# Kernel optimization log

Hardware: AMD Instinct MI355X
Metric: run time of the kernel (lower is better)

Reference implementation:

```python
import jax, jax.numpy as jnp
import numpy as np

B, DL, DC, DG = 4, 64, 64, 64
NL, NC = 8192, 16384
SLOPE = 0.01  # LeakyReLU default negative_slope


def _lin(x, W, b):
    # 1x1 Conv1d == per-node linear: x [B, in, N] -> [B, out, N]
    return jnp.einsum('oi,bin->bon', W, x) + b[None, :, None]


def _leaky(x):
    return jnp.where(x >= 0, x, SLOPE * x)


def _flip(L):
    # swap first and second half along last dim (literal <-> complement)
    n = L.shape[-1]
    return jnp.concatenate([L[..., n // 2:], L[..., :n // 2]], axis=-1)


def setup_inputs() -> dict:
    key = jax.random.key(0)
    ks = jax.random.split(key, 14)
    L_t = jax.random.normal(ks[0], (B, DL, NL), dtype=jnp.float32)
    C_t = jax.random.normal(ks[1], (B, DC, NC), dtype=jnp.float32)
    U_t = jax.random.normal(ks[2], (B, DG, 1), dtype=jnp.float32)
    # sparse 0/1 adjacency, ~8 literals per clause
    A = (jax.random.uniform(ks[3], (NC, NL)) < 0.001).astype(jnp.float32)
    A_t = A.T
    s = 0.05
    W_Lmsg = s * jax.random.normal(ks[4], (DC, DL));      b_Lmsg = jnp.zeros((DC,))
    W_Cmsg = s * jax.random.normal(ks[5], (DL, DC));      b_Cmsg = jnp.zeros((DL,))
    W_Lu   = s * jax.random.normal(ks[6], (DL, 3 * DL));  b_Lu   = jnp.zeros((DL,))
    W_Cu   = s * jax.random.normal(ks[7], (DC, 2 * DC));  b_Cu   = jnp.zeros((DC,))
    W_Uu   = s * jax.random.normal(ks[8], (DG, DL + DC + DG)); b_Uu = jnp.zeros((DG,))
    return dict(L_t=L_t, C_t=C_t, U_t=U_t, A=A, A_t=A_t,
                W_Lmsg=W_Lmsg, b_Lmsg=b_Lmsg, W_Cmsg=W_Cmsg, b_Cmsg=b_Cmsg,
                W_Lu=W_Lu, b_Lu=b_Lu, W_Cu=W_Cu, b_Cu=b_Cu, W_Uu=W_Uu, b_Uu=b_Uu)


def reference(L_t, C_t, U_t, A, A_t,
              W_Lmsg, b_Lmsg, W_Cmsg, b_Cmsg,
              W_Lu, b_Lu, W_Cu, b_Cu, W_Uu, b_Uu):
    # literal -> clause messages: [B, d_c, n_lits] @ [n_lits, n_clauses]
    M_l = _lin(L_t, W_Lmsg, b_Lmsg) @ A_t
    C_t_new = _leaky(_lin(jnp.concatenate([C_t, M_l], axis=1), W_Cu, b_Cu))
    # clause -> literal messages: [B, d_l, n_clauses] @ [n_clauses, n_lits]
    M_c = _lin(C_t_new, W_Cmsg, b_Cmsg) @ A
    L_t_new = _leaky(_lin(jnp.concatenate([L_t, M_c, _flip(L_t)], axis=1), W_Lu, b_Lu))
    glob = jnp.concatenate([L_t_new.sum(-1, keepdims=True),
                            C_t_new.sum(-1, keepdims=True), U_t], axis=1)
    U_t_new = _leaky(_lin(glob, W_Uu, b_Uu))
    return (L_t_new, C_t_new, U_t_new)
```

## Files before the change

### kernel.cpp

```cpp
#include <hip/hip_runtime.h>

#define NLIT 8192
#define NCLS 16384
#define DD 64
#define CCAP 64
#define LCAP 64

__device__ __forceinline__ float leaky(float x){ return x >= 0.f ? x : 0.01f*x; }

__device__ __forceinline__ int sel4(int g, int4 li){
  return g==0 ? li.x : (g==1 ? li.y : (g==2 ? li.z : li.w));
}

__device__ __forceinline__ float bf2f(unsigned short u){
  unsigned v = ((unsigned)u) << 16;
  union { unsigned u; float f; } c; c.u = v; return c.f;
}
__device__ __forceinline__ unsigned short f2bf(float f){
  union { float f; unsigned u; } c; c.f = f;
  unsigned b = c.u + 0x7fffu + ((c.u >> 16) & 1u);
  return (unsigned short)(b >> 16);
}

__global__ __launch_bounds__(256) void extract_lmsg_k(const uint4* __restrict__ A4,
    int* __restrict__ ccnt, int* __restrict__ clist,
    int* __restrict__ lcnt, int* __restrict__ llist,
    const float* __restrict__ L, const float* __restrict__ W,
    const float* __restrict__ bias, unsigned short* __restrict__ LmsgT){
  if (blockIdx.x < 16384){
    const int T = 16384*256;
    int tid = blockIdx.x*256 + threadIdx.x;
    uint4 v[8];
    #pragma unroll
    for (int u=0;u<8;u++) v[u] = A4[tid + (size_t)u*T];
    #pragma unroll
    for (int u=0;u<8;u++){
      if (v[u].x | v[u].y | v[u].z | v[u].w){
        int i = tid + u*T;
        int c = i >> 11;
        int l = (i & 2047) << 2;
        unsigned vv[4] = {v[u].x, v[u].y, v[u].z, v[u].w};
        #pragma unroll
        for (int j=0;j<4;j++){
          if (vv[j]){
            int p = atomicAdd(&ccnt[c],1);
            if (p < CCAP) clist[c*CCAP+p] = l+j;
            int q = atomicAdd(&lcnt[l+j],1);
            if (q < LCAP) llist[(l+j)*LCAP+q] = c;
          }
        }
      }
    }
  } else {
    __shared__ float X[64][65];
    __shared__ float Y[64][65];
    int bid = blockIdx.x - 16384;
    int b   = (bid & 7) >> 1;
    int l0  = (((bid >> 3) << 1) | (bid & 1)) << 6;
    int lane = threadIdx.x & 63;
    int wg = __builtin_amdgcn_readfirstlane(threadIdx.x >> 6);
    const float* Lb = L + (size_t)b*DD*NLIT;
    #pragma unroll
    for (int r=0;r<16;r++){
      int i = wg + 4*r;
      X[lane][i] = Lb[(size_t)i*NLIT + l0 + lane];
    }
    __syncthreads();
    float acc[16];
    #pragma unroll
    for (int j=0;j<16;j++) acc[j] = bias[wg*16+j];
    #pragma unroll 4
    for (int i=0;i<64;i++){
      float x = X[lane][i];
      #pragma unroll
      for (int j=0;j<16;j++) acc[j] += W[(wg*16+j)*64+i] * x;
    }
    #pragma unroll
    for (int j=0;j<16;j++) Y[lane][wg*16+j] = acc[j];
    __syncthreads();
    unsigned short* out = LmsgT + ((size_t)b*NLIT + l0)*64;
    #pragma unroll
    for (int r=0;r<16;r++){
      int cc = wg + 4*r;
      out[cc*64 + lane] = f2bf(Y[cc][lane]);
    }
  }
}

__device__ __forceinline__ void gather_grp4(const unsigned short* __restrict__ src,
    const int* __restrict__ list, int cap, const int* kk, int lane,
    float (* __restrict__ sb)[65], int row0){
  int g = lane >> 4;
  int h = lane & 15;
  float4 a0={0.f,0.f,0.f,0.f}, a1=a0, a2=a0, a3=a0;
  int r0=(kk[0]+3)>>2, r1=(kk[1]+3)>>2, r2=(kk[2]+3)>>2, r3=(kk[3]+3)>>2;
  int Rm = max(max(r0,r1),max(r2,r3));
  for (int r=0;r<Rm;r++){
    if (r<r0){ int4 li=*(const int4*)&list[0*cap+4*r]; int e=4*r+g; bool vd=e<kk[0];
      int idx=vd?sel4(g,li):0; ushort4 x=*(const ushort4*)&src[(size_t)idx*64+4*h];
      if(vd){ a0.x+=bf2f(x.x); a0.y+=bf2f(x.y); a0.z+=bf2f(x.z); a0.w+=bf2f(x.w); } }
    if (r<r1){ int4 li=*(const int4*)&list[1*cap+4*r]; int e=4*r+g; bool vd=e<kk[1];
      int idx=vd?sel4(g,li):0; ushort4 x=*(const ushort4*)&src[(size_t)idx*64+4*h];
      if(vd){ a1.x+=bf2f(x.x); a1.y+=bf2f(x.y); a1.z+=bf2f(x.z); a1.w+=bf2f(x.w); } }
    if (r<r2){ int4 li=*(const int4*)&list[2*cap+4*r]; int e=4*r+g; bool vd=e<kk[2];
      int idx=vd?sel4(g,li):0; ushort4 x=*(const ushort4*)&src[(size_t)idx*64+4*h];
      if(vd){ a2.x+=bf2f(x.x); a2.y+=bf2f(x.y); a2.z+=bf2f(x.z); a2.w+=bf2f(x.w); } }
    if (r<r3){ int4 li=*(const int4*)&list[3*cap+4*r]; int e=4*r+g; bool vd=e<kk[3];
      int idx=vd?sel4(g,li):0; ushort4 x=*(const ushort4*)&src[(size_t)idx*64+4*h];
      if(vd){ a3.x+=bf2f(x.x); a3.y+=bf2f(x.y); a3.z+=bf2f(x.z); a3.w+=bf2f(x.w); } }
  }
  #pragma unroll
  for (int s=16;s<=32;s<<=1){
    a0.x+=__shfl_xor(a0.x,s,64); a0.y+=__shfl_xor(a0.y,s,64); a0.z+=__shfl_xor(a0.z,s,64); a0.w+=__shfl_xor(a0.w,s,64);
    a1.x+=__shfl_xor(a1.x,s,64); a1.y+=__shfl_xor(a1.y,s,64); a1.z+=__shfl_xor(a1.z,s,64); a1.w+=__shfl_xor(a1.w,s,64);
    a2.x+=__shfl_xor(a2.x,s,64); a2.y+=__shfl_xor(a2.y,s,64); a2.z+=__shfl_xor(a2.z,s,64); a2.w+=__shfl_xor(a2.w,s,64);
    a3.x+=__shfl_xor(a3.x,s,64); a3.y+=__shfl_xor(a3.y,s,64); a3.z+=__shfl_xor(a3.z,s,64); a3.w+=__shfl_xor(a3.w,s,64);
  }
  sb[row0+0][4*h+g] = g==0?a0.x:(g==1?a0.y:(g==2?a0.z:a0.w));
  sb[row0+1][4*h+g] = g==0?a1.x:(g==1?a1.y:(g==2?a1.z:a1.w));
  sb[row0+2][4*h+g] = g==0?a2.x:(g==1?a2.y:(g==2?a2.z:a2.w));
  sb[row0+3][4*h+g] = g==0?a3.x:(g==1?a3.y:(g==2?a3.z:a3.w));
}

__global__ __launch_bounds__(512) void clause_k(const float* __restrict__ Ct,
    const unsigned short* __restrict__ LmsgT, const int* __restrict__ ccnt, const int* __restrict__ clist,
    const float* __restrict__ W_Cu, const float* __restrict__ b_Cu,
    const float* __restrict__ W_Cmsg, const float* __restrict__ b_Cmsg,
    unsigned short* __restrict__ CmsgT, float* __restrict__ outC){
  __shared__ float SA[64][65];
  __shared__ float SB[64][65];
  int bx = blockIdx.x;
  int b  = (bx & 7) >> 1;
  int c0 = (((bx >> 3) << 1) | (bx & 1)) << 6;
  int lane = threadIdx.x & 63;
  int wg = __builtin_amdgcn_readfirstlane(threadIdx.x >> 6);
  int kk[8];
  #pragma unroll
  for (int t=0;t<8;t++){
    int k = ccnt[c0 + wg*8 + t];
    kk[t] = k > CCAP ? CCAP : k;
  }
  const float* Cb = Ct + (size_t)b*DD*NCLS;
  #pragma unroll
  for (int r=0;r<8;r++){
    int i = wg + 8*r;
    SA[lane][i] = Cb[(size_t)i*NCLS + c0 + lane];
  }
  const unsigned short* Lm = LmsgT + (size_t)b*NLIT*64;
  #pragma unroll
  for (int tg=0;tg<2;tg++){
    int row0 = wg*8 + tg*4;
    gather_grp4(Lm, &clist[(c0+row0)*CCAP], CCAP, &kk[tg*4], lane, SB, row0);
  }
  __syncthreads();
  float v[8];
  {
    float acc[8];
    #pragma unroll
    for (int j=0;j<8;j++) acc[j] = b_Cu[wg*8+j];
    #pragma unroll 4
    for (int i=0;i<64;i++){
      float xa = SA[lane][i];
      float xm = SB[lane][i];
      #pragma unroll
      for (int j=0;j<8;j++){
        int o = wg*8+j;
        acc[j] += W_Cu[o*128+i]*xa + W_Cu[o*128+64+i]*xm;
      }
    }
    #pragma unroll
    for (int j=0;j<8;j++) v[j] = leaky(acc[j]);
  }
  float* oC = outC + (size_t)b*DD*NCLS;
  #pragma unroll
  for (int j=0;j<8;j++){
    int o = wg*8+j;
    oC[(size_t)o*NCLS + c0 + lane] = v[j];
  }
  __syncthreads();
  #pragma unroll
  for (int j=0;j<8;j++) SB[lane][wg*8+j] = v[j];
  __syncthreads();
  float acc2[8];
  #pragma unroll
  for (int j=0;j<8;j++) acc2[j] = b_Cmsg[wg*8+j];
  #pragma unroll 4
  for (int i=0;i<64;i++){
    float x = SB[lane][i];
    #pragma unroll
    for (int j=0;j<8;j++) acc2[j] += W_Cmsg[(wg*8+j)*64+i]*x;
  }
  #pragma unroll
  for (int j=0;j<8;j++) SA[lane][wg*8+j] = acc2[j];
  __syncthreads();
  unsigned short* oM = CmsgT + ((size_t)b*NCLS + c0)*64;
  #pragma unroll
  for (int r=0;r<8;r++){
    int cc = wg + 8*r;
    oM[cc*64 + lane] = f2bf(SA[cc][lane]);
  }
}

__global__ __launch_bounds__(512) void literal_redc_k(const float* __restrict__ Lt,
    const unsigned short* __restrict__ CmsgT, const int* __restrict__ lcnt, const int* __restrict__ llist,
    const float* __restrict__ W_Lu, const float* __restrict__ b_Lu,
    float* __restrict__ outL, const float* __restrict__ outC, float* __restrict__ Csum){
  if (blockIdx.x >= 512){
    __shared__ float red[8];
    int r = blockIdx.x - 512;
    int t = threadIdx.x;
    float s = 0.f;
    const float4* p = (const float4*)(outC + (size_t)r*NCLS);
    #pragma unroll
    for (int i=0;i<8;i++){
      float4 v = p[t + 512*i];
      s += v.x + v.y + v.z + v.w;
    }
    #pragma unroll
    for (int sft=32;sft>0;sft>>=1) s += __shfl_xor(s, sft, 64);
    if ((t & 63) == 0) red[t >> 6] = s;
    __syncthreads();
    if (t == 0){
      float tot = 0.f;
      #pragma unroll
      for (int i=0;i<8;i++) tot += red[i];
      Csum[r] = tot;
    }
    return;
  }
  __shared__ float SX[64][65];
  __shared__ float SF[64][65];
  __shared__ float SM[64][65];
  int bx = blockIdx.x;
  int b  = (bx & 7) >> 1;
  int l0 = (((bx >> 3) << 1) | (bx & 1)) << 6;
  int lane = threadIdx.x & 63;
  int wg = __builtin_amdgcn_readfirstlane(threadIdx.x >> 6);
  int kk[8];
  #pragma unroll
  for (int t=0;t<8;t++){
    int k = lcnt[l0 + wg*8 + t];
    kk[t] = k > LCAP ? LCAP : k;
  }
  const float* Lb = Lt + (size_t)b*DD*NLIT;
  int f0 = l0 ^ 4096;
  #pragma unroll
  for (int r=0;r<8;r++){
    int i = wg + 8*r;
    SX[lane][i] = Lb[(size_t)i*NLIT + l0 + lane];
    SF[lane][i] = Lb[(size_t)i*NLIT + f0 + lane];
  }
  const unsigned short* Cm = CmsgT + (size_t)b*NCLS*64;
  #pragma unroll
  for (int tg=0;tg<2;tg++){
    int row0 = wg*8 + tg*4;
    gather_grp4(Cm, &llist[(l0+row0)*LCAP], LCAP, &kk[tg*4], lane, SM, row0);
  }
  __syncthreads();
  float acc[8];
  #pragma unroll
  for (int j=0;j<8;j++) acc[j] = b_Lu[wg*8+j];
  #pragma unroll 4
  for (int i=0;i<64;i++){
    float xx = SX[lane][i], xm = SM[lane][i], xf = SF[lane][i];
    #pragma unroll
    for (int j=0;j<8;j++){
      int o = wg*8+j;
      acc[j] += W_Lu[o*192+i]*xx + W_Lu[o*192+64+i]*xm + W_Lu[o*192+128+i]*xf;
    }
  }
  float* oL = outL + (size_t)b*DD*NLIT;
  #pragma unroll
  for (int j=0;j<8;j++){
    int o = wg*8+j;
    oL[(size_t)o*NLIT + l0 + lane] = leaky(acc[j]);
  }
}

__global__ __launch_bounds__(256) void redl_k(const float* __restrict__ outL,
    float* __restrict__ Lsum){
  __shared__ float red[4];
  int r = blockIdx.x;
  int t = threadIdx.x;
  float s = 0.f;
  const float4* p = (const float4*)(outL + (size_t)r*NLIT);
  #pragma unroll
  for (int i=0;i<8;i++){
    float4 v = p[t + 256*i];
    s += v.x + v.y + v.z + v.w;
  }
  #pragma unroll
  for (int sft=32;sft>0;sft>>=1) s += __shfl_xor(s, sft, 64);
  if ((t & 63) == 0) red[t >> 6] = s;
  __syncthreads();
  if (t == 0) Lsum[r] = red[0] + red[1] + red[2] + red[3];
}

__global__ void u_k(const float* __restrict__ Lsum, const float* __restrict__ Csum,
                    const float* __restrict__ Ut, const float* __restrict__ W,
                    const float* __restrict__ bias, float* __restrict__ outU){
  int t = threadIdx.x;
  int b = t >> 6, o = t & 63;
  float acc = bias[o];
  for (int i=0;i<64;i++){
    acc += W[o*192+i]*Lsum[b*64+i] + W[o*192+64+i]*Csum[b*64+i] + W[o*192+128+i]*Ut[b*64+i];
  }
  outU[t] = leaky(acc);
}

extern "C" void kernel_launch(void* const* d_in, const int* in_sizes, int n_in,
                              void* d_out, int out_size, void* d_ws, size_t ws_size,
                              hipStream_t stream){
  (void)in_sizes; (void)n_in; (void)out_size; (void)ws_size;
  const float* L_t    = (const float*)d_in[0];
  const float* C_t    = (const float*)d_in[1];
  const float* U_t    = (const float*)d_in[2];
  const float* A      = (const float*)d_in[3];
  const float* W_Lmsg = (const float*)d_in[5];
  const float* b_Lmsg = (const float*)d_in[6];
  const float* W_Cmsg = (const float*)d_in[7];
  const float* b_Cmsg = (const float*)d_in[8];
  const float* W_Lu   = (const float*)d_in[9];
  const float* b_Lu   = (const float*)d_in[10];
  const float* W_Cu   = (const float*)d_in[11];
  const float* b_Cu   = (const float*)d_in[12];
  const float* W_Uu   = (const float*)d_in[13];
  const float* b_Uu   = (const float*)d_in[14];

  char* ws = (char*)d_ws;
  unsigned short* LmsgT = (unsigned short*)ws;
  unsigned short* CmsgT = (unsigned short*)(ws + 4194304);
  int*   ccnt  = (int*)  (ws + 12582912);
  int*   lcnt  = (int*)  (ws + 12648448);
  float* Lsum  = (float*)(ws + 12681216);
  float* Csum  = (float*)(ws + 12682240);
  int*   clist = (int*)  (ws + 12683264);
  int*   llist = (int*)  (ws + 16877568);

  hipMemsetAsync(ws + 12582912, 0, 98304, stream);

  float* outL = (float*)d_out;
  float* outC = (float*)d_out + 2097152;
  float* outU = (float*)d_out + 6291456;

  extract_lmsg_k<<<16896, 256, 0, stream>>>((const uint4*)A, ccnt, clist, lcnt, llist,
                                            L_t, W_Lmsg, b_Lmsg, LmsgT);
  clause_k      <<<1024,  512, 0, stream>>>(C_t, LmsgT, ccnt, clist, W_Cu, b_Cu,
                                            W_Cmsg, b_Cmsg, CmsgT, outC);
  literal_redc_k<<<768,   512, 0, stream>>>(L_t, CmsgT, lcnt, llist, W_Lu, b_Lu,
                                            outL, outC, Csum);
  redl_k        <<<256,   256, 0, stream>>>(outL, Lsum);
  u_k           <<<1,     256, 0, stream>>>(Lsum, Csum, U_t, W_Uu, b_Uu, outU);
}
```

Before: 1.044 ms.

## Interleave batch dimension into message buffers so gathers fetch all batches at once

The literal and clause message buffers change from batch-major [B][N][64] to node-major [N][B*64]. Each neighbour index now fetches one contiguous 512-byte row covering all four batches, so every wave reads each adjacency list once instead of once per batch, and the loads are wide and coalesced. The clause and literal kernels are retiled to match: 32 clauses or 16 literals across all batches per block, with matching shared-memory layouts. Clause-side gathered sums are now kept in shared memory as bf16, which adds an extra rounding step.

```diff
diff --git a/kernel.cpp b/kernel.cpp
--- a/kernel.cpp
+++ b/kernel.cpp
@@ -8,13 +8,8 @@
 
 __device__ __forceinline__ float leaky(float x){ return x >= 0.f ? x : 0.01f*x; }
 
-__device__ __forceinline__ int sel4(int g, int4 li){
-  return g==0 ? li.x : (g==1 ? li.y : (g==2 ? li.z : li.w));
-}
-
 __device__ __forceinline__ float bf2f(unsigned short u){
-  unsigned v = ((unsigned)u) << 16;
-  union { unsigned u; float f; } c; c.u = v; return c.f;
+  union { unsigned u; float f; } c; c.u = ((unsigned)u) << 16; return c.f;
 }
 __device__ __forceinline__ unsigned short f2bf(float f){
   union { float f; unsigned u; } c; c.f = f;
@@ -26,7 +21,7 @@
     int* __restrict__ ccnt, int* __restrict__ clist,
     int* __restrict__ lcnt, int* __restrict__ llist,
     const float* __restrict__ L, const float* __restrict__ W,
-    const float* __restrict__ bias, unsigned short* __restrict__ LmsgT){
+    const float* __restrict__ bias, unsigned short* __restrict__ LmsgT2){
   if (blockIdx.x < 16384){
     const int T = 16384*256;
     int tid = blockIdx.x*256 + threadIdx.x;
@@ -55,8 +50,8 @@
     __shared__ float X[64][65];
     __shared__ float Y[64][65];
     int bid = blockIdx.x - 16384;
-    int b   = (bid & 7) >> 1;
-    int l0  = (((bid >> 3) << 1) | (bid & 1)) << 6;
+    int b   = bid >> 7;
+    int l0  = (bid & 127) << 6;
     int lane = threadIdx.x & 63;
     int wg = __builtin_amdgcn_readfirstlane(threadIdx.x >> 6);
     const float* Lb = L + (size_t)b*DD*NLIT;
@@ -78,131 +73,130 @@
     #pragma unroll
     for (int j=0;j<16;j++) Y[lane][wg*16+j] = acc[j];
     __syncthreads();
-    unsigned short* out = LmsgT + ((size_t)b*NLIT + l0)*64;
     #pragma unroll
     for (int r=0;r<16;r++){
       int cc = wg + 4*r;
-      out[cc*64 + lane] = f2bf(Y[cc][lane]);
-    }
-  }
-}
-
-__device__ __forceinline__ void gather_grp4(const unsigned short* __restrict__ src,
-    const int* __restrict__ list, int cap, const int* kk, int lane,
-    float (* __restrict__ sb)[65], int row0){
-  int g = lane >> 4;
-  int h = lane & 15;
-  float4 a0={0.f,0.f,0.f,0.f}, a1=a0, a2=a0, a3=a0;
-  int r0=(kk[0]+3)>>2, r1=(kk[1]+3)>>2, r2=(kk[2]+3)>>2, r3=(kk[3]+3)>>2;
-  int Rm = max(max(r0,r1),max(r2,r3));
-  for (int r=0;r<Rm;r++){
-    if (r<r0){ int4 li=*(const int4*)&list[0*cap+4*r]; int e=4*r+g; bool vd=e<kk[0];
-      int idx=vd?sel4(g,li):0; ushort4 x=*(const ushort4*)&src[(size_t)idx*64+4*h];
-      if(vd){ a0.x+=bf2f(x.x); a0.y+=bf2f(x.y); a0.z+=bf2f(x.z); a0.w+=bf2f(x.w); } }
-    if (r<r1){ int4 li=*(const int4*)&list[1*cap+4*r]; int e=4*r+g; bool vd=e<kk[1];
-      int idx=vd?sel4(g,li):0; ushort4 x=*(const ushort4*)&src[(size_t)idx*64+4*h];
-      if(vd){ a1.x+=bf2f(x.x); a1.y+=bf2f(x.y); a1.z+=bf2f(x.z); a1.w+=bf2f(x.w); } }
-    if (r<r2){ int4 li=*(const int4*)&list[2*cap+4*r]; int e=4*r+g; bool vd=e<kk[2];
-      int idx=vd?sel4(g,li):0; ushort4 x=*(const ushort4*)&src[(size_t)idx*64+4*h];
-      if(vd){ a2.x+=bf2f(x.x); a2.y+=bf2f(x.y); a2.z+=bf2f(x.z); a2.w+=bf2f(x.w); } }
-    if (r<r3){ int4 li=*(const int4*)&list[3*cap+4*r]; int e=4*r+g; bool vd=e<kk[3];
-      int idx=vd?sel4(g,li):0; ushort4 x=*(const ushort4*)&src[(size_t)idx*64+4*h];
-      if(vd){ a3.x+=bf2f(x.x); a3.y+=bf2f(x.y); a3.z+=bf2f(x.z); a3.w+=bf2f(x.w); } }
-  }
-  #pragma unroll
-  for (int s=16;s<=32;s<<=1){
-    a0.x+=__shfl_xor(a0.x,s,64); a0.y+=__shfl_xor(a0.y,s,64); a0.z+=__shfl_xor(a0.z,s,64); a0.w+=__shfl_xor(a0.w,s,64);
-    a1.x+=__shfl_xor(a1.x,s,64); a1.y+=__shfl_xor(a1.y,s,64); a1.z+=__shfl_xor(a1.z,s,64); a1.w+=__shfl_xor(a1.w,s,64);
-    a2.x+=__shfl_xor(a2.x,s,64); a2.y+=__shfl_xor(a2.y,s,64); a2.z+=__shfl_xor(a2.z,s,64); a2.w+=__shfl_xor(a2.w,s,64);
-    a3.x+=__shfl_xor(a3.x,s,64); a3.y+=__shfl_xor(a3.y,s,64); a3.z+=__shfl_xor(a3.z,s,64); a3.w+=__shfl_xor(a3.w,s,64);
-  }
-  sb[row0+0][4*h+g] = g==0?a0.x:(g==1?a0.y:(g==2?a0.z:a0.w));
-  sb[row0+1][4*h+g] = g==0?a1.x:(g==1?a1.y:(g==2?a1.z:a1.w));
-  sb[row0+2][4*h+g] = g==0?a2.x:(g==1?a2.y:(g==2?a2.z:a2.w));
-  sb[row0+3][4*h+g] = g==0?a3.x:(g==1?a3.y:(g==2?a3.z:a3.w));
+      LmsgT2[(size_t)(l0+cc)*256 + b*64 + lane] = f2bf(Y[cc][lane]);
+    }
+  }
 }
 
 __global__ __launch_bounds__(512) void clause_k(const float* __restrict__ Ct,
-    const unsigned short* __restrict__ LmsgT, const int* __restrict__ ccnt, const int* __restrict__ clist,
+    const unsigned short* __restrict__ LmsgT2, const int* __restrict__ ccnt,
+    const int* __restrict__ clist,
     const float* __restrict__ W_Cu, const float* __restrict__ b_Cu,
     const float* __restrict__ W_Cmsg, const float* __restrict__ b_Cmsg,
-    unsigned short* __restrict__ CmsgT, float* __restrict__ outC){
-  __shared__ float SA[64][65];
-  __shared__ float SB[64][65];
-  int bx = blockIdx.x;
-  int b  = (bx & 7) >> 1;
-  int c0 = (((bx >> 3) << 1) | (bx & 1)) << 6;
+    unsigned short* __restrict__ CmsgT2, float* __restrict__ outC){
+  __shared__ float SA[4][64][33];
+  __shared__ unsigned short SB[4][32][66];
+  int c0 = blockIdx.x << 5;
   int lane = threadIdx.x & 63;
-  int wg = __builtin_amdgcn_readfirstlane(threadIdx.x >> 6);
-  int kk[8];
-  #pragma unroll
-  for (int t=0;t<8;t++){
-    int k = ccnt[c0 + wg*8 + t];
-    kk[t] = k > CCAP ? CCAP : k;
-  }
-  const float* Cb = Ct + (size_t)b*DD*NCLS;
-  #pragma unroll
-  for (int r=0;r<8;r++){
-    int i = wg + 8*r;
-    SA[lane][i] = Cb[(size_t)i*NCLS + c0 + lane];
-  }
-  const unsigned short* Lm = LmsgT + (size_t)b*NLIT*64;
-  #pragma unroll
-  for (int tg=0;tg<2;tg++){
-    int row0 = wg*8 + tg*4;
-    gather_grp4(Lm, &clist[(c0+row0)*CCAP], CCAP, &kk[tg*4], lane, SB, row0);
-  }
-  __syncthreads();
-  float v[8];
-  {
-    float acc[8];
-    #pragma unroll
-    for (int j=0;j<8;j++) acc[j] = b_Cu[wg*8+j];
+  int w = __builtin_amdgcn_readfirstlane(threadIdx.x >> 6);
+  #pragma unroll
+  for (int it=0; it<16; it++){
+    int row = w*32 + it*2 + (lane>>5);
+    int b = row >> 6, i = row & 63;
+    SA[b][i][lane&31] = Ct[((size_t)b*64 + i)*NCLS + c0 + (lane&31)];
+  }
+  {
+    int kk[4], rT[4];
+    #pragma unroll
+    for (int t=0;t<4;t++){
+      int k = ccnt[c0 + w*4 + t];
+      kk[t] = k > CCAP ? CCAP : k;
+      rT[t] = (kk[t]+3) >> 2;
+    }
+    int Rm = max(max(rT[0],rT[1]),max(rT[2],rT[3]));
+    float4 acc[4];
+    #pragma unroll
+    for (int t=0;t<4;t++) acc[t] = make_float4(0.f,0.f,0.f,0.f);
+    for (int r=0;r<Rm;r++){
+      #pragma unroll
+      for (int t=0;t<4;t++){
+        if (r < rT[t]){
+          int4 li = *(const int4*)&clist[(c0 + w*4 + t)*CCAP + 4*r];
+          int idx[4] = {li.x, li.y, li.z, li.w};
+          #pragma unroll
+          for (int e=0;e<4;e++){
+            if (4*r+e < kk[t]){
+              ushort4 x = *(const ushort4*)&LmsgT2[(size_t)idx[e]*256 + 4*lane];
+              acc[t].x += bf2f(x.x); acc[t].y += bf2f(x.y);
+              acc[t].z += bf2f(x.z); acc[t].w += bf2f(x.w);
+            }
+          }
+        }
+      }
+    }
+    int b = lane >> 4, h = lane & 15;
+    #pragma unroll
+    for (int t=0;t<4;t++){
+      SB[b][w*4+t][4*h+0] = f2bf(acc[t].x);
+      SB[b][w*4+t][4*h+1] = f2bf(acc[t].y);
+      SB[b][w*4+t][4*h+2] = f2bf(acc[t].z);
+      SB[b][w*4+t][4*h+3] = f2bf(acc[t].w);
+    }
+  }
+  __syncthreads();
+  int b = w >> 1, half = w & 1, cl = lane & 31, sub = lane >> 5;
+  float acc[16];
+  {
+    int ob = half*32 + sub*16;
+    #pragma unroll
+    for (int j=0;j<16;j++) acc[j] = b_Cu[ob+j];
     #pragma unroll 4
     for (int i=0;i<64;i++){
-      float xa = SA[lane][i];
-      float xm = SB[lane][i];
-      #pragma unroll
-      for (int j=0;j<8;j++){
-        int o = wg*8+j;
+      float xa = SA[b][i][cl];
+      float xm = bf2f(SB[b][cl][i]);
+      #pragma unroll
+      for (int j=0;j<16;j++){
+        int o = ob + j;
         acc[j] += W_Cu[o*128+i]*xa + W_Cu[o*128+64+i]*xm;
       }
     }
     #pragma unroll
-    for (int j=0;j<8;j++) v[j] = leaky(acc[j]);
-  }
-  float* oC = outC + (size_t)b*DD*NCLS;
-  #pragma unroll
-  for (int j=0;j<8;j++){
-    int o = wg*8+j;
-    oC[(size_t)o*NCLS + c0 + lane] = v[j];
-  }
-  __syncthreads();
-  #pragma unroll
-  for (int j=0;j<8;j++) SB[lane][wg*8+j] = v[j];
-  __syncthreads();
-  float acc2[8];
-  #pragma unroll
-  for (int j=0;j<8;j++) acc2[j] = b_Cmsg[wg*8+j];
-  #pragma unroll 4
-  for (int i=0;i<64;i++){
-    float x = SB[lane][i];
-    #pragma unroll
-    for (int j=0;j<8;j++) acc2[j] += W_Cmsg[(wg*8+j)*64+i]*x;
-  }
-  #pragma unroll
-  for (int j=0;j<8;j++) SA[lane][wg*8+j] = acc2[j];
-  __syncthreads();
-  unsigned short* oM = CmsgT + ((size_t)b*NCLS + c0)*64;
-  #pragma unroll
-  for (int r=0;r<8;r++){
-    int cc = wg + 8*r;
-    oM[cc*64 + lane] = f2bf(SA[cc][lane]);
+    for (int j=0;j<16;j++) acc[j] = leaky(acc[j]);
+    float* oC = outC + (size_t)b*DD*NCLS;
+    #pragma unroll
+    for (int j=0;j<16;j++) oC[(size_t)(ob+j)*NCLS + c0 + cl] = acc[j];
+  }
+  __syncthreads();
+  {
+    int ob = half*32 + sub*16;
+    #pragma unroll
+    for (int j=0;j<16;j++) SA[b][ob+j][cl] = acc[j];
+  }
+  __syncthreads();
+  float acc2[16];
+  {
+    int ob = half*32 + sub*16;
+    #pragma unroll
+    for (int j=0;j<16;j++) acc2[j] = b_Cmsg[ob+j];
+    #pragma unroll 4
+    for (int i=0;i<64;i++){
+      float x = SA[b][i][cl];
+      #pragma unroll
+      for (int j=0;j<16;j++) acc2[j] += W_Cmsg[(ob+j)*64+i]*x;
+    }
+    #pragma unroll
+    for (int j=0;j<16;j++) SB[b][cl][ob+j] = f2bf(acc2[j]);
+  }
+  __syncthreads();
+  {
+    int bb = lane >> 4, h = lane & 15;
+    #pragma unroll
+    for (int t=0;t<4;t++){
+      int cc = w*4 + t;
+      ushort4 x;
+      x.x = SB[bb][cc][4*h+0]; x.y = SB[bb][cc][4*h+1];
+      x.z = SB[bb][cc][4*h+2]; x.w = SB[bb][cc][4*h+3];
+      *(ushort4*)&CmsgT2[(size_t)(c0+cc)*256 + 4*lane] = x;
+    }
   }
 }
 
 __global__ __launch_bounds__(512) void literal_redc_k(const float* __restrict__ Lt,
-    const unsigned short* __restrict__ CmsgT, const int* __restrict__ lcnt, const int* __restrict__ llist,
+    const unsigned short* __restrict__ CmsgT2, const int* __restrict__ lcnt,
+    const int* __restrict__ llist,
     const float* __restrict__ W_Lu, const float* __restrict__ b_Lu,
     float* __restrict__ outL, const float* __restrict__ outC, float* __restrict__ Csum){
   if (blockIdx.x >= 512){
@@ -228,53 +222,79 @@
     }
     return;
   }
-  __shared__ float SX[64][65];
-  __shared__ float SF[64][65];
-  __shared__ float SM[64][65];
-  int bx = blockIdx.x;
-  int b  = (bx & 7) >> 1;
-  int l0 = (((bx >> 3) << 1) | (bx & 1)) << 6;
+  __shared__ float SX[4][64][17];
+  __shared__ float SF[4][64][17];
+  __shared__ float SM[4][16][65];
+  int l0 = blockIdx.x << 4;
+  int f0 = l0 ^ 4096;
   int lane = threadIdx.x & 63;
-  int wg = __builtin_amdgcn_readfirstlane(threadIdx.x >> 6);
-  int kk[8];
-  #pragma unroll
-  for (int t=0;t<8;t++){
-    int k = lcnt[l0 + wg*8 + t];
-    kk[t] = k > LCAP ? LCAP : k;
-  }
-  const float* Lb = Lt + (size_t)b*DD*NLIT;
-  int f0 = l0 ^ 4096;
-  #pragma unroll
-  for (int r=0;r<8;r++){
-    int i = wg + 8*r;
-    SX[lane][i] = Lb[(size_t)i*NLIT + l0 + lane];
-    SF[lane][i] = Lb[(size_t)i*NLIT + f0 + lane];
-  }
-  const unsigned short* Cm = CmsgT + (size_t)b*NCLS*64;
-  #pragma unroll
-  for (int tg=0;tg<2;tg++){
-    int row0 = wg*8 + tg*4;
-    gather_grp4(Cm, &llist[(l0+row0)*LCAP], LCAP, &kk[tg*4], lane, SM, row0);
-  }
-  __syncthreads();
+  int w = __builtin_amdgcn_readfirstlane(threadIdx.x >> 6);
+  #pragma unroll
+  for (int it=0; it<8; it++){
+    int row = w*32 + it*4 + (lane>>4);
+    int b = row >> 6, i = row & 63;
+    int col = lane & 15;
+    SX[b][i][col] = Lt[((size_t)b*64 + i)*NLIT + l0 + col];
+    SF[b][i][col] = Lt[((size_t)b*64 + i)*NLIT + f0 + col];
+  }
+  {
+    int kk[2], rT[2];
+    #pragma unroll
+    for (int t=0;t<2;t++){
+      int k = lcnt[l0 + w*2 + t];
+      kk[t] = k > LCAP ? LCAP : k;
+      rT[t] = (kk[t]+3) >> 2;
+    }
+    int Rm = max(rT[0], rT[1]);
+    float4 acc[2];
+    #pragma unroll
+    for (int t=0;t<2;t++) acc[t] = make_float4(0.f,0.f,0.f,0.f);
+    for (int r=0;r<Rm;r++){
+      #pragma unroll
+      for (int t=0;t<2;t++){
+        if (r < rT[t]){
+          int4 li = *(const int4*)&llist[(l0 + w*2 + t)*LCAP + 4*r];
+          int idx[4] = {li.x, li.y, li.z, li.w};
+          #pragma unroll
+          for (int e=0;e<4;e++){
+            if (4*r+e < kk[t]){
+              ushort4 x = *(const ushort4*)&CmsgT2[(size_t)idx[e]*256 + 4*lane];
+              acc[t].x += bf2f(x.x); acc[t].y += bf2f(x.y);
+              acc[t].z += bf2f(x.z); acc[t].w += bf2f(x.w);
+            }
+          }
+        }
+      }
+    }
+    int b = lane >> 4, h = lane & 15;
+    #pragma unroll
+    for (int t=0;t<2;t++){
+      SM[b][w*2+t][4*h+0] = acc[t].x;
+      SM[b][w*2+t][4*h+1] = acc[t].y;
+      SM[b][w*2+t][4*h+2] = acc[t].z;
+      SM[b][w*2+t][4*h+3] = acc[t].w;
+    }
+  }
+  __syncthreads();
+  int b = w >> 1, half = w & 1, cl = lane & 15, sub = lane >> 4;
+  int ob = half*32 + sub*8;
   float acc[8];
   #pragma unroll
-  for (int j=0;j<8;j++) acc[j] = b_Lu[wg*8+j];
+  for (int j=0;j<8;j++) acc[j] = b_Lu[ob+j];
   #pragma unroll 4
   for (int i=0;i<64;i++){
-    float xx = SX[lane][i], xm = SM[lane][i], xf = SF[lane][i];
+    float xx = SX[b][i][cl];
+    float xm = SM[b][cl][i];
+    float xf = SF[b][i][cl];
     #pragma unroll
     for (int j=0;j<8;j++){
-      int o = wg*8+j;
+      int o = ob + j;
       acc[j] += W_Lu[o*192+i]*xx + W_Lu[o*192+64+i]*xm + W_Lu[o*192+128+i]*xf;
     }
   }
   float* oL = outL + (size_t)b*DD*NLIT;
   #pragma unroll
-  for (int j=0;j<8;j++){
-    int o = wg*8+j;
-    oL[(size_t)o*NLIT + l0 + lane] = leaky(acc[j]);
-  }
+  for (int j=0;j<8;j++) oL[(size_t)(ob+j)*NLIT + l0 + cl] = leaky(acc[j]);
 }
 
 __global__ __launch_bounds__(256) void redl_k(const float* __restrict__ outL,
@@ -328,8 +348,8 @@
   const float* b_Uu   = (const float*)d_in[14];
 
   char* ws = (char*)d_ws;
-  unsigned short* LmsgT = (unsigned short*)ws;
-  unsigned short* CmsgT = (unsigned short*)(ws + 4194304);
+  unsigned short* LmsgT2 = (unsigned short*)ws;
+  unsigned short* CmsgT2 = (unsigned short*)(ws + 4194304);
   int*   ccnt  = (int*)  (ws + 12582912);
   int*   lcnt  = (int*)  (ws + 12648448);
   float* Lsum  = (float*)(ws + 12681216);
@@ -344,10 +364,10 @@
   float* outU = (float*)d_out + 6291456;
 
   extract_lmsg_k<<<16896, 256, 0, stream>>>((const uint4*)A, ccnt, clist, lcnt, llist,
-                                            L_t, W_Lmsg, b_Lmsg, LmsgT);
-  clause_k      <<<1024,  512, 0, stream>>>(C_t, LmsgT, ccnt, clist, W_Cu, b_Cu,
-                                            W_Cmsg, b_Cmsg, CmsgT, outC);
-  literal_redc_k<<<768,   512, 0, stream>>>(L_t, CmsgT, lcnt, llist, W_Lu, b_Lu,
+                                            L_t, W_Lmsg, b_Lmsg, LmsgT2);
+  clause_k      <<<512,   512, 0, stream>>>(C_t, LmsgT2, ccnt, clist, W_Cu, b_Cu,
+                                            W_Cmsg, b_Cmsg, CmsgT2, outC);
+  literal_redc_k<<<768,   512, 0, stream>>>(L_t, CmsgT2, lcnt, llist, W_Lu, b_Lu,
                                             outL, outC, Csum);
   redl_k        <<<256,   256, 0, stream>>>(outL, Lsum);
   u_k           <<<1,     256, 0, stream>>>(Lsum, Csum, U_t, W_Uu, b_Uu, outU);
```

Result: slower. 1.146 ms (+9.8%).
